# Kernel optimization log

Hardware: AMD Instinct MI355X
Metric: run time of the kernel (lower is better)

Reference implementation:

```python
import jax, jax.numpy as jnp
import numpy as np

H = 7      # n_hazards
B = 8      # batch
S = 2048   # seq_len
D = 768    # hidden_dim
K = 64     # bottleneck_dim
THR = 0.05 # influence_threshold


def setup_inputs() -> dict:
    key = jax.random.key(0)
    k0, k1, k2, k3 = jax.random.split(key, 4)
    x = jax.random.normal(k0, (H, B, S, D), jnp.float32)          # stacked hazard reprs
    M = jax.random.normal(k1, (H, H), jnp.float32) * 0.3           # interaction_matrix [src, tgt]
    W1 = jax.random.normal(k2, (H, H, D, K), jnp.float32) * (1.0 / np.sqrt(D).astype(np.float32))
    b1 = jnp.zeros((H, H, K), jnp.float32)
    W2 = jax.random.normal(k3, (H, H, K, D), jnp.float32) * (1.0 / np.sqrt(K).astype(np.float32))
    b2 = jnp.zeros((H, H, D), jnp.float32)
    return {"x": x, "M": M, "W1": W1, "b1": b1, "W2": W2, "b2": b2}


def reference(x, M, W1, b1, W2, b2):
    # Gate: influence used only if |M[s,t]| > threshold and s != t (torch skips the
    # projection entirely below threshold; masking to 0 yields identical values/grads).
    eye = jnp.eye(H, dtype=bool)
    gate = jnp.where((jnp.abs(M) > THR) & (~eye), M, jnp.zeros_like(M))  # [s, t]

    # Bottleneck MLP for all (source, target) pairs in one batched GEMM.
    # h: [s, t, b, n, k]
    h = jnp.einsum('sbnd,stdk->stbnk', x, W1) + b1[:, :, None, None, :]
    h = jax.nn.gelu(h, approximate=False)  # torch nn.GELU default is exact (erf)

    # Fold the scalar gate into the second GEMM so the [s,t,b,n,D] tensor is never
    # materialized; sum over sources lands directly at each target.
    add = jnp.einsum('st,stbnk,stkd->tbnd', gate, h, W2)
    add = add + jnp.einsum('st,std->td', gate, b2)[:, None, None, :]
    return x + add  # [H, B, S, D] stacked in hazard order
```

## Files before the change

### kernel.cpp

```cpp
#include <hip/hip_runtime.h>
#include <hip/hip_bf16.h>
#include <math.h>

#define NH   7
#define NROW 16384
#define DD   768
#define KK   64
#define THRG 0.05f

typedef float  f32x4   __attribute__((ext_vector_type(4)));
typedef __bf16 bf16x8  __attribute__((ext_vector_type(8)));
typedef short  short8v __attribute__((ext_vector_type(8)));
typedef short  short4v __attribute__((ext_vector_type(4)));

union V8 { short8v s; bf16x8 b; };

__device__ __forceinline__ float gate_of(const float* __restrict__ M, int s, int t) {
  float m = M[s * NH + t];
  return (s != t && fabsf(m) > THRG) ? m : 0.0f;
}

__device__ __forceinline__ float gelu_t(float v) {
  float u = 0.7978845608028654f * (v + 0.044715f * v * v * v);
  return v / (1.0f + __expf(-2.0f * u));
}

__device__ __forceinline__ void gload_lds16(const void* g, void* l) {
  __builtin_amdgcn_global_load_lds(
      (const __attribute__((address_space(1))) unsigned int*)g,
      (__attribute__((address_space(3))) unsigned int*)l, 16, 0, 0);
}

__global__ void prep_w1(const float* __restrict__ W1, unsigned short* __restrict__ W1P) {
  int pr = blockIdx.x;
  const float* src = W1 + (size_t)pr * DD * KK;
  __bf16* dst = (__bf16*)(W1P + (size_t)pr * 12 * 4096);
  for (int idx = threadIdx.x; idx < 12 * 4096; idx += blockDim.x) {
    int kc = idx >> 12, rem = idx & 4095;
    int kcol = rem >> 6, dl = rem & 63;
    int dl_log = dl ^ ((kcol & 7) << 3);
    dst[idx] = (__bf16)src[(size_t)(kc * 64 + dl_log) * KK + kcol];
  }
}

__global__ void prep_w2(const float* __restrict__ M, const float* __restrict__ W2,
                        unsigned short* __restrict__ W2P) {
  int st = blockIdx.x;
  int s = st / NH, t = st % NH;
  float g = gate_of(M, s, t);
  const float* src = W2 + (size_t)st * KK * DD;
  __bf16* dst = (__bf16*)(W2P + (size_t)((t * NH + s) * 6) * 8192);
  for (int idx = threadIdx.x; idx < 6 * 128 * 64; idx += blockDim.x) {
    int nb = idx >> 13, rem = idx & 8191;
    int dloc = rem >> 6, k = rem & 63;
    dst[idx] = (__bf16)(g * src[(size_t)k * DD + nb * 128 + dloc]);
  }
}

__global__ void prep_b2(const float* __restrict__ M, const float* __restrict__ b2,
                        float* __restrict__ b2sum) {
  int idx = blockIdx.x * blockDim.x + threadIdx.x;
  if (idx >= NH * DD) return;
  int t = idx / DD, d = idx % DD;
  float acc = 0.f;
  for (int s = 0; s < NH; ++s)
    acc += gate_of(M, s, t) * b2[(size_t)(s * NH + t) * DD + d];
  b2sum[idx] = acc;
}

__global__ __launch_bounds__(256)
void chiA(const float* __restrict__ x, const float* __restrict__ M,
          const unsigned short* __restrict__ W1P, const float* __restrict__ b1,
          unsigned short* __restrict__ H) {
  __shared__ __align__(16) unsigned short xs[128 * 64];
  __shared__ __align__(16) unsigned short w1s0[64 * 64];
  __shared__ __align__(16) unsigned short w1s1[64 * 64];

  int bid = (int)blockIdx.x;
  int nid = (bid & 7) * 448 + (bid >> 3);
  int tg = nid & 3;  int rem = nid >> 2;
  int s = rem % NH, rb = rem / NH;
  int t0 = tg * 2, t1 = tg * 2 + 1;
  float g0 = gate_of(M, s, t0);
  float g1 = (t1 < NH) ? gate_of(M, s, t1) : 0.0f;
  bool a0 = (g0 != 0.0f), a1 = (g1 != 0.0f);
  if (!a0 && !a1) return;
  int pr0 = s * NH + t0, pr1 = s * NH + t1;
  int row0 = rb * 128;

  int tid = (int)threadIdx.x;
  int wid = tid >> 6, lane = tid & 63, l16 = lane & 15, l4 = lane >> 4;

  const f32x4 zero = {0.f, 0.f, 0.f, 0.f};
  f32x4 acc0[4][2], acc1[4][2];
#pragma unroll
  for (int m = 0; m < 4; ++m)
#pragma unroll
    for (int n = 0; n < 2; ++n) { acc0[m][n] = zero; acc1[m][n] = zero; }

  const float* xb = x + ((size_t)s * NROW + row0) * DD;
  const char* w1b0 = (const char*)(W1P + (size_t)pr0 * 12 * 4096);
  const char* w1b1 = (const char*)(W1P + (size_t)pr1 * 12 * 4096);

  for (int kc = 0; kc < 12; ++kc) {
    __syncthreads();
    if (a0) {
      const char* wsrc = w1b0 + (size_t)kc * 8192;
      char* wdst = (char*)w1s0 + (wid << 10);
#pragma unroll
      for (int r = 0; r < 2; ++r)
        gload_lds16(wsrc + r * 4096 + tid * 16, wdst + r * 4096);
    }
    if (a1) {
      const char* wsrc = w1b1 + (size_t)kc * 8192;
      char* wdst = (char*)w1s1 + (wid << 10);
#pragma unroll
      for (int r = 0; r < 2; ++r)
        gload_lds16(wsrc + r * 4096 + tid * 16, wdst + r * 4096);
    }
#pragma unroll
    for (int r = 0; r < 4; ++r) {
      int L = r * 4096 + tid * 16;
      int row = L >> 7, colB = L & 127;
      const float* gp = xb + (size_t)row * DD + kc * 64 + (colB >> 1);
      f32x4 v0 = *(const f32x4*)gp;
      f32x4 v1 = *(const f32x4*)(gp + 4);
      bf16x8 sv;
      sv[0] = (__bf16)v0[0]; sv[1] = (__bf16)v0[1];
      sv[2] = (__bf16)v0[2]; sv[3] = (__bf16)v0[3];
      sv[4] = (__bf16)v1[0]; sv[5] = (__bf16)v1[1];
      sv[6] = (__bf16)v1[2]; sv[7] = (__bf16)v1[3];
      *(bf16x8*)((char*)xs + (L ^ ((row & 7) << 4))) = sv;
    }
    __syncthreads();

    V8 bf2[2][2];
#pragma unroll
    for (int nn = 0; nn < 2; ++nn)
#pragma unroll
      for (int k2 = 0; k2 < 2; ++k2) {
        int xr = wid * 32 + nn * 16 + l16;
        int byte = (xr * 128 + k2 * 64 + l4 * 16) ^ ((xr & 7) << 4);
        bf2[nn][k2].s = *(const short8v*)((const char*)xs + byte);
      }
    if (a0) {
      V8 af[4][2];
#pragma unroll
      for (int mm = 0; mm < 4; ++mm)
#pragma unroll
        for (int k2 = 0; k2 < 2; ++k2) {
          int rowl = mm * 16 + l16;
          int byte = (rowl * 128 + k2 * 64 + l4 * 16) ^ ((rowl & 7) << 4);
          af[mm][k2].s = *(const short8v*)((const char*)w1s0 + byte);
        }
#pragma unroll
      for (int k2 = 0; k2 < 2; ++k2)
#pragma unroll
        for (int mm = 0; mm < 4; ++mm)
#pragma unroll
          for (int nn = 0; nn < 2; ++nn)
            acc0[mm][nn] = __builtin_amdgcn_mfma_f32_16x16x32_bf16(af[mm][k2].b, bf2[nn][k2].b, acc0[mm][nn], 0, 0, 0);
    }
    if (a1) {
      V8 af[4][2];
#pragma unroll
      for (int mm = 0; mm < 4; ++mm)
#pragma unroll
        for (int k2 = 0; k2 < 2; ++k2) {
          int rowl = mm * 16 + l16;
          int byte = (rowl * 128 + k2 * 64 + l4 * 16) ^ ((rowl & 7) << 4);
          af[mm][k2].s = *(const short8v*)((const char*)w1s1 + byte);
        }
#pragma unroll
      for (int k2 = 0; k2 < 2; ++k2)
#pragma unroll
        for (int mm = 0; mm < 4; ++mm)
#pragma unroll
          for (int nn = 0; nn < 2; ++nn)
            acc1[mm][nn] = __builtin_amdgcn_mfma_f32_16x16x32_bf16(af[mm][k2].b, bf2[nn][k2].b, acc1[mm][nn], 0, 0, 0);
    }
  }

  if (a0) {
#pragma unroll
    for (int mm = 0; mm < 4; ++mm) {
      f32x4 bv = *(const f32x4*)(b1 + (size_t)pr0 * KK + mm * 16 + l4 * 4);
#pragma unroll
      for (int nn = 0; nn < 2; ++nn) {
        union { short4v s4; __bf16 b4[4]; } o;
#pragma unroll
        for (int r = 0; r < 4; ++r) o.b4[r] = (__bf16)gelu_t(acc0[mm][nn][r] + bv[r]);
        int xrow = row0 + wid * 32 + nn * 16 + l16;
        unsigned short* hp = H + ((size_t)pr0 * NROW + xrow) * KK + mm * 16 + l4 * 4;
        *(short4v*)hp = o.s4;
      }
    }
  }
  if (a1) {
#pragma unroll
    for (int mm = 0; mm < 4; ++mm) {
      f32x4 bv = *(const f32x4*)(b1 + (size_t)pr1 * KK + mm * 16 + l4 * 4);
#pragma unroll
      for (int nn = 0; nn < 2; ++nn) {
        union { short4v s4; __bf16 b4[4]; } o;
#pragma unroll
        for (int r = 0; r < 4; ++r) o.b4[r] = (__bf16)gelu_t(acc1[mm][nn][r] + bv[r]);
        int xrow = row0 + wid * 32 + nn * 16 + l16;
        unsigned short* hp = H + ((size_t)pr1 * NROW + xrow) * KK + mm * 16 + l4 * 4;
        *(short4v*)hp = o.s4;
      }
    }
  }
}

__global__ __launch_bounds__(256)
void chiB(const unsigned short* __restrict__ H, const float* __restrict__ x,
          const float* __restrict__ M, const unsigned short* __restrict__ W2P,
          const float* __restrict__ b2sum, float* __restrict__ out) {
  __shared__ __align__(16) unsigned short hs[128 * 64];

  int bid = (int)blockIdx.x;
  int nid = (bid & 7) * 672 + (bid >> 3);
  int nb = nid % 6, rem = nid / 6;
  int rb = rem % 128, t = rem / 128;
  int row0 = rb * 128, col0 = nb * 128;

  int tid = (int)threadIdx.x;
  int wid = tid >> 6, lane = tid & 63, l16 = lane & 15, l4 = lane >> 4;
  int wr = wid & 1, wc = wid >> 1;

  const f32x4 zero = {0.f, 0.f, 0.f, 0.f};
  f32x4 acc[4][4];
#pragma unroll
  for (int m = 0; m < 4; ++m)
#pragma unroll
    for (int n = 0; n < 4; ++n) acc[m][n] = zero;

  for (int s = 0; s < NH; ++s) {
    if (gate_of(M, s, t) == 0.0f) continue;

    const char* wb = (const char*)(W2P + (size_t)((t * NH + s) * 6 + nb) * 8192);
    V8 af[4][2];
#pragma unroll
    for (int m = 0; m < 4; ++m)
#pragma unroll
      for (int k2 = 0; k2 < 2; ++k2) {
        int dl = wc * 64 + m * 16 + l16;
        af[m][k2].s = *(const short8v*)(wb + dl * 128 + k2 * 64 + l4 * 16);
      }

    __syncthreads();
    const char* hb = (const char*)(H + ((size_t)(s * NH + t) * NROW + row0) * KK);
#pragma unroll
    for (int r = 0; r < 4; ++r) {
      int L = r * 4096 + tid * 16;
      int row = L >> 7;
      short8v v = *(const short8v*)(hb + L);
      *(short8v*)((char*)hs + (L ^ ((row & 7) << 4))) = v;
    }
    __syncthreads();

    V8 bfr[4][2];
#pragma unroll
    for (int n = 0; n < 4; ++n)
#pragma unroll
      for (int k2 = 0; k2 < 2; ++k2) {
        int rl = wr * 64 + n * 16 + l16;
        int byte = (rl * 128 + k2 * 64 + l4 * 16) ^ ((rl & 7) << 4);
        bfr[n][k2].s = *(const short8v*)((const char*)hs + byte);
      }
#pragma unroll
    for (int k2 = 0; k2 < 2; ++k2)
#pragma unroll
      for (int m = 0; m < 4; ++m)
#pragma unroll
        for (int n = 0; n < 4; ++n)
          acc[m][n] = __builtin_amdgcn_mfma_f32_16x16x32_bf16(af[m][k2].b, bfr[n][k2].b, acc[m][n], 0, 0, 0);
  }

#pragma unroll
  for (int m = 0; m < 4; ++m) {
    int col = col0 + wc * 64 + m * 16 + l4 * 4;
    f32x4 bv = *(const f32x4*)(b2sum + (size_t)t * DD + col);
#pragma unroll
    for (int n = 0; n < 4; ++n) {
      int row = row0 + wr * 64 + n * 16 + l16;
      size_t off = ((size_t)t * NROW + row) * DD + col;
      f32x4 xv = *(const f32x4*)(x + off);
      f32x4 ov;
#pragma unroll
      for (int r = 0; r < 4; ++r) ov[r] = acc[m][n][r] + xv[r] + bv[r];
      *(f32x4*)(out + off) = ov;
    }
  }
}

extern "C" void kernel_launch(void* const* d_in, const int* in_sizes, int n_in,
                              void* d_out, int out_size, void* d_ws, size_t ws_size,
                              hipStream_t stream) {
  const float* x  = (const float*)d_in[0];
  const float* M  = (const float*)d_in[1];
  const float* W1 = (const float*)d_in[2];
  const float* b1 = (const float*)d_in[3];
  const float* W2 = (const float*)d_in[4];
  const float* b2 = (const float*)d_in[5];
  float* out = (float*)d_out;

  char* ws = (char*)d_ws;
  unsigned short* W1P = (unsigned short*)ws;
  unsigned short* W2P = (unsigned short*)(ws + 4816896);
  float* b2sum        = (float*)(ws + 9633792);
  unsigned short* H   = (unsigned short*)(ws + 9655296);

  prep_w1<<<dim3(49), dim3(256), 0, stream>>>(W1, W1P);
  prep_w2<<<dim3(49), dim3(256), 0, stream>>>(M, W2, W2P);
  prep_b2<<<dim3((NH * DD + 255) / 256), dim3(256), 0, stream>>>(M, b2, b2sum);
  chiA<<<dim3(3584), dim3(256), 0, stream>>>(x, M, W1P, b1, H);
  chiB<<<dim3(5376), dim3(256), 0, stream>>>(H, x, M, W2P, b2sum, out);
}
```

Measured before the change: 544.3 us.

## Double-buffer H and W2 tiles in chiB via direct global-to-LDS loads

chiA now writes H in a pre-swizzled tile layout and prep_w2 pre-swizzles W2P, so chiB can stream both operands into LDS with direct global-to-LDS 16-byte loads. The loads for the next source are issued before the MFMA work on the current one, using two LDS buffers. This is meant to hide global-load latency and remove the register round trip through VGPRs. It doubles LDS use, which may lower occupancy, and it depends on a gload_lds16 helper and hand-placed waitcnt and barrier ordering.

```diff
diff --git a/kernel.cpp b/kernel.cpp
--- a/kernel.cpp
+++ b/kernel.cpp
@@ -53,7 +53,8 @@
   for (int idx = threadIdx.x; idx < 6 * 128 * 64; idx += blockDim.x) {
     int nb = idx >> 13, rem = idx & 8191;
     int dloc = rem >> 6, k = rem & 63;
-    dst[idx] = (__bf16)(g * src[(size_t)k * DD + nb * 128 + dloc]);
+    int k_log = k ^ ((dloc & 7) << 3);
+    dst[idx] = (__bf16)(g * src[(size_t)k_log * DD + nb * 128 + dloc]);
   }
 }
 
@@ -182,6 +183,7 @@
   }
 
   if (a0) {
+    unsigned short* Hb = H + ((size_t)pr0 * 128 + rb) * 8192;
 #pragma unroll
     for (int mm = 0; mm < 4; ++mm) {
       f32x4 bv = *(const f32x4*)(b1 + (size_t)pr0 * KK + mm * 16 + l4 * 4);
@@ -190,13 +192,13 @@
         union { short4v s4; __bf16 b4[4]; } o;
 #pragma unroll
         for (int r = 0; r < 4; ++r) o.b4[r] = (__bf16)gelu_t(acc0[mm][nn][r] + bv[r]);
-        int xrow = row0 + wid * 32 + nn * 16 + l16;
-        unsigned short* hp = H + ((size_t)pr0 * NROW + xrow) * KK + mm * 16 + l4 * 4;
-        *(short4v*)hp = o.s4;
+        int rl = wid * 32 + nn * 16 + l16;
+        *(short4v*)((char*)Hb + ((rl * 128 + mm * 32 + l4 * 8) ^ ((rl & 7) << 4))) = o.s4;
       }
     }
   }
   if (a1) {
+    unsigned short* Hb = H + ((size_t)pr1 * 128 + rb) * 8192;
 #pragma unroll
     for (int mm = 0; mm < 4; ++mm) {
       f32x4 bv = *(const f32x4*)(b1 + (size_t)pr1 * KK + mm * 16 + l4 * 4);
@@ -205,9 +207,8 @@
         union { short4v s4; __bf16 b4[4]; } o;
 #pragma unroll
         for (int r = 0; r < 4; ++r) o.b4[r] = (__bf16)gelu_t(acc1[mm][nn][r] + bv[r]);
-        int xrow = row0 + wid * 32 + nn * 16 + l16;
-        unsigned short* hp = H + ((size_t)pr1 * NROW + xrow) * KK + mm * 16 + l4 * 4;
-        *(short4v*)hp = o.s4;
+        int rl = wid * 32 + nn * 16 + l16;
+        *(short4v*)((char*)Hb + ((rl * 128 + mm * 32 + l4 * 8) ^ ((rl & 7) << 4))) = o.s4;
       }
     }
   }
@@ -217,7 +218,8 @@
 void chiB(const unsigned short* __restrict__ H, const float* __restrict__ x,
           const float* __restrict__ M, const unsigned short* __restrict__ W2P,
           const float* __restrict__ b2sum, float* __restrict__ out) {
-  __shared__ __align__(16) unsigned short hs[128 * 64];
+  __shared__ __align__(16) unsigned short hsbuf[2][128 * 64];
+  __shared__ __align__(16) unsigned short w2buf[2][128 * 64];
 
   int bid = (int)blockIdx.x;
   int nid = (bid & 7) * 672 + (bid >> 3);
@@ -229,6 +231,12 @@
   int wid = tid >> 6, lane = tid & 63, l16 = lane & 15, l4 = lane >> 4;
   int wr = wid & 1, wc = wid >> 1;
 
+  unsigned spack = 0; int nact = 0;
+  for (int s = 0; s < NH; ++s) {
+    if (s == t) continue;
+    if (fabsf(M[s * NH + t]) > THRG) { spack |= (unsigned)s << (3 * nact); ++nact; }
+  }
+
   const f32x4 zero = {0.f, 0.f, 0.f, 0.f};
   f32x4 acc[4][4];
 #pragma unroll
@@ -236,46 +244,64 @@
 #pragma unroll
     for (int n = 0; n < 4; ++n) acc[m][n] = zero;
 
-  for (int s = 0; s < NH; ++s) {
-    if (gate_of(M, s, t) == 0.0f) continue;
-
-    const char* wb = (const char*)(W2P + (size_t)((t * NH + s) * 6 + nb) * 8192);
-    V8 af[4][2];
-#pragma unroll
-    for (int m = 0; m < 4; ++m)
-#pragma unroll
-      for (int k2 = 0; k2 < 2; ++k2) {
-        int dl = wc * 64 + m * 16 + l16;
-        af[m][k2].s = *(const short8v*)(wb + dl * 128 + k2 * 64 + l4 * 16);
+  auto STAGE = [&](int i, int p) {
+    int s = (spack >> (3 * i)) & 7;
+    const char* hsrc = (const char*)H + ((size_t)(s * NH + t) * 128 + rb) * 16384;
+    const char* wsrc = (const char*)W2P + (size_t)((t * NH + s) * 6 + nb) * 16384;
+    char* hdst = (char*)(&hsbuf[p][0]) + (wid << 10);
+    char* wdst = (char*)(&w2buf[p][0]) + (wid << 10);
+#pragma unroll
+    for (int r = 0; r < 4; ++r) {
+      gload_lds16(hsrc + r * 4096 + tid * 16, hdst + r * 4096);
+      gload_lds16(wsrc + r * 4096 + tid * 16, wdst + r * 4096);
+    }
+  };
+
+  if (nact > 0) {
+    STAGE(0, 0);
+    for (int i = 0; i < nact; ++i) {
+      int p = i & 1;
+      if (i + 1 < nact) {
+        STAGE(i + 1, p ^ 1);
+        asm volatile("s_waitcnt vmcnt(8)" ::: "memory");
+      } else {
+        asm volatile("s_waitcnt vmcnt(0)" ::: "memory");
       }
-
-    __syncthreads();
-    const char* hb = (const char*)(H + ((size_t)(s * NH + t) * NROW + row0) * KK);
-#pragma unroll
-    for (int r = 0; r < 4; ++r) {
-      int L = r * 4096 + tid * 16;
-      int row = L >> 7;
-      short8v v = *(const short8v*)(hb + L);
-      *(short8v*)((char*)hs + (L ^ ((row & 7) << 4))) = v;
-    }
-    __syncthreads();
-
-    V8 bfr[4][2];
-#pragma unroll
-    for (int n = 0; n < 4; ++n)
-#pragma unroll
-      for (int k2 = 0; k2 < 2; ++k2) {
-        int rl = wr * 64 + n * 16 + l16;
-        int byte = (rl * 128 + k2 * 64 + l4 * 16) ^ ((rl & 7) << 4);
-        bfr[n][k2].s = *(const short8v*)((const char*)hs + byte);
-      }
-#pragma unroll
-    for (int k2 = 0; k2 < 2; ++k2)
+      __builtin_amdgcn_s_barrier();
+      __builtin_amdgcn_sched_barrier(0);
+
+      const char* hsp = (const char*)(&hsbuf[p][0]);
+      const char* w2p = (const char*)(&w2buf[p][0]);
+      V8 af[4][2], bfr[4][2];
 #pragma unroll
       for (int m = 0; m < 4; ++m)
 #pragma unroll
-        for (int n = 0; n < 4; ++n)
-          acc[m][n] = __builtin_amdgcn_mfma_f32_16x16x32_bf16(af[m][k2].b, bfr[n][k2].b, acc[m][n], 0, 0, 0);
+        for (int k2 = 0; k2 < 2; ++k2) {
+          int dl = wc * 64 + m * 16 + l16;
+          int byte = (dl * 128 + k2 * 64 + l4 * 16) ^ ((dl & 7) << 4);
+          af[m][k2].s = *(const short8v*)(w2p + byte);
+        }
+#pragma unroll
+      for (int n = 0; n < 4; ++n)
+#pragma unroll
+        for (int k2 = 0; k2 < 2; ++k2) {
+          int rl = wr * 64 + n * 16 + l16;
+          int byte = (rl * 128 + k2 * 64 + l4 * 16) ^ ((rl & 7) << 4);
+          bfr[n][k2].s = *(const short8v*)(hsp + byte);
+        }
+#pragma unroll
+      for (int k2 = 0; k2 < 2; ++k2)
+#pragma unroll
+        for (int m = 0; m < 4; ++m)
+#pragma unroll
+          for (int n = 0; n < 4; ++n)
+            acc[m][n] = __builtin_amdgcn_mfma_f32_16x16x32_bf16(af[m][k2].b, bfr[n][k2].b, acc[m][n], 0, 0, 0);
+
+      asm volatile("s_waitcnt lgkmcnt(0)" ::: "memory");
+      __builtin_amdgcn_sched_barrier(0);
+      __builtin_amdgcn_s_barrier();
+      __builtin_amdgcn_sched_barrier(0);
+    }
   }
 
 #pragma unroll
```

New measurement: 458.1 us. -15.8%, faster.
